# Kernel optimization log

Measured on AMD Instinct MI355X. Metric: run time of the kernel, lower is better.

The kernel has to match this reference:

```python
import jax, jax.numpy as jnp
import numpy as np

N_ORDER = 256
BATCH = 512
SEQ_LEN = 4096


def make_legs_matrices(N):
    # HiPPO-LegS: A[n,k] = -sqrt(2n+1)sqrt(2k+1) for n>k, -(n+1) for n==k, 0 for n<k
    # B[n] = sqrt(2n+1)
    q = np.arange(N, dtype=np.float64)
    r = np.sqrt(2.0 * q + 1.0)
    M = r[:, None] * r[None, :] * (q[:, None] > q[None, :]).astype(np.float64)
    M = M + np.diag(q + 1.0)
    A = -M
    B = r[:, None]
    return jnp.asarray(A, jnp.float32), jnp.asarray(B, jnp.float32)


def setup_inputs() -> dict:
    key = jax.random.key(0)
    A, Bm = make_legs_matrices(N_ORDER)
    f = jax.random.normal(key, (BATCH, SEQ_LEN), dtype=jnp.float32)
    init_state = jnp.zeros((BATCH, 1, N_ORDER), dtype=jnp.float32)
    return {"f": f, "A": A, "Bm": Bm, "init_state": init_state}


def reference(f, A, Bm, init_state):
    # Generalized bilinear transform discretization, alpha = 0.5, step = 1.0
    step = 1.0
    alpha = 0.5
    N = A.shape[0]
    I = jnp.eye(N, dtype=A.dtype)
    inv_step = 1.0 / step
    part1 = I - inv_step * alpha * A
    part2 = I + inv_step * (1.0 - alpha) * A
    # Original uses lstsq; part1 is nonsingular so solve is equivalent.
    Ad = jnp.linalg.solve(part1, part2)            # (N, N)
    Bd = jnp.linalg.solve(part1, inv_step * Bm)    # (N, 1)

    BdT = Bd.T[None]  # (1, 1, N)

    def step_fn(c, f_k):
        # c: (B, 1, N), f_k: (B,)
        # c_k = c_{k-1} @ Ad^T + Bd^T * f_k
        c = jnp.einsum('bin,mn->bim', c, Ad) + BdT * f_k[:, None, None]
        return c, None

    # scan over time axis; batch fully vectorized inside each step
    c_k, _ = jax.lax.scan(step_fn, init_state, jnp.swapaxes(f, 0, 1))
    return c_k  # (B, 1, N)
```

## Files before the change

kernel.cpp:

```cpp
#include <hip/hip_runtime.h>

#define NORD 256
#define TLEN 4096
#define NBATCH 512

__device__ __forceinline__ void fill_T2(float (*dst)[72], const float* __restrict__ s0,
                                        const float* __restrict__ s1, int stride, int t) {
  const int r = t & 63, qq = t >> 6;
  const float* p0 = s0 + (size_t)r * stride + 4 * qq;
  float4 v = *reinterpret_cast<const float4*>(p0);
  float4 w = *reinterpret_cast<const float4*>(p0 + 16);
  if (s1) {
    const float* p1 = s1 + (size_t)r * stride + 4 * qq;
    const float4 v1 = *reinterpret_cast<const float4*>(p1);
    const float4 w1 = *reinterpret_cast<const float4*>(p1 + 16);
    v.x += v1.x; v.y += v1.y; v.z += v1.z; v.w += v1.w;
    w.x += w1.x; w.y += w1.y; w.z += w1.z; w.w += w1.w;
  }
  dst[4 * qq + 0][r] = v.x;  dst[4 * qq + 1][r] = v.y;
  dst[4 * qq + 2][r] = v.z;  dst[4 * qq + 3][r] = v.w;
  dst[4 * qq + 16][r] = w.x; dst[4 * qq + 17][r] = w.y;
  dst[4 * qq + 18][r] = w.z; dst[4 * qq + 19][r] = w.w;
}

__device__ __forceinline__ void fill_N2(float (*dst)[72], const float* __restrict__ s0,
                                        const float* __restrict__ s1, int stride, int t) {
  const int kk = t >> 3, c8 = (t & 7) << 3;
  const float* p0 = s0 + (size_t)kk * stride + c8;
  float4 v = *reinterpret_cast<const float4*>(p0);
  float4 w = *reinterpret_cast<const float4*>(p0 + 4);
  if (s1) {
    const float* p1 = s1 + (size_t)kk * stride + c8;
    const float4 v1 = *reinterpret_cast<const float4*>(p1);
    const float4 w1 = *reinterpret_cast<const float4*>(p1 + 4);
    v.x += v1.x; v.y += v1.y; v.z += v1.z; v.w += v1.w;
    w.x += w1.x; w.y += w1.y; w.z += w1.z; w.w += w1.w;
  }
  dst[kk][c8 + 0] = v.x; dst[kk][c8 + 1] = v.y; dst[kk][c8 + 2] = v.z; dst[kk][c8 + 3] = v.w;
  dst[kk][c8 + 4] = w.x; dst[kk][c8 + 5] = w.y; dst[kk][c8 + 6] = w.z; dst[kk][c8 + 7] = w.w;
}

__device__ __forceinline__ void tile_fma4(const float (*As)[72], const float (*Bs)[72],
                                          int tr, int tc, float acc[4][4]) {
#pragma unroll
  for (int k = 0; k < 32; ++k) {
    const float4 a4 = *reinterpret_cast<const float4*>(&As[k][4 * tr]);
    const float4 b4 = *reinterpret_cast<const float4*>(&Bs[k][4 * tc]);
    const float a[4] = {a4.x, a4.y, a4.z, a4.w};
    const float b[4] = {b4.x, b4.y, b4.z, b4.w};
#pragma unroll
    for (int ii = 0; ii < 4; ++ii)
#pragma unroll
      for (int jj = 0; jj < 4; ++jj)
        acc[ii][jj] += a[ii] * b[jj];
  }
}

__global__ __launch_bounds__(256) void k_inv(const float* __restrict__ A,
                                             const float* __restrict__ Bm,
                                             float* __restrict__ P00, float* P01,
                                             float* __restrict__ U0, float* U1) {
  const int bid = blockIdx.x;
  const int i = threadIdx.x;
  const int wave = i >> 6, lane = i & 63;
  __shared__ float xs[NORD];
  float b = (bid < NORD) ? ((i == bid) ? 1.0f : 0.0f) : Bm[i];
  const float invd = 1.0f / (1.0f - 0.5f * A[i * NORD + i]);
  for (int w = 0; w < 4; ++w) {
    if (wave == w) {
      const int base = w << 6;
      for (int jj = 0; jj < 64; ++jj) {
        float bj = __shfl(b, jj);
        float dj = __shfl(invd, jj);
        float xj = bj * dj;
        if (lane > jj) {
          b += 0.5f * A[i * NORD + base + jj] * xj;
        } else if (lane == jj) {
          b = xj;
        }
      }
      xs[i] = b;
    }
    __syncthreads();
    if (wave > w) {
      const int base = w << 6;
      const float4* arow = reinterpret_cast<const float4*>(A + i * NORD + base);
#pragma unroll
      for (int q = 0; q < 16; ++q) {
        float4 a4 = arow[q];
        b += 0.5f * (a4.x * xs[base + 4 * q + 0] + a4.y * xs[base + 4 * q + 1] +
                     a4.z * xs[base + 4 * q + 2] + a4.w * xs[base + 4 * q + 3]);
      }
    }
  }
  if (bid < NORD) {
    P00[i * NORD + bid] = 2.0f * b - ((i == bid) ? 1.0f : 0.0f);
    if (P01) P01[(size_t)bid * 256 + i] = 0.0f;
  } else {
    U0[i] = b;
    if (U1) U1[i] = 0.0f;
  }
}

__global__ __launch_bounds__(256) void k_stage(float* U0, float* U1,
                                               const float* Pin0, const float* Pin1,
                                               float* Pout0, float* Pout1,
                                               int J, int n_apply) {
  const int bid = blockIdx.x;
  const int t = threadIdx.x;
  const int tr = t >> 4, tc = t & 15;
  __shared__ float As[32][72];
  __shared__ float Bs[32][72];
  const int kspan = U1 ? 128 : 256;

  if (bid < n_apply) {
    int work = bid, ks = 0;
    if (U1) { ks = work & 1; work >>= 1; }
    const int j0 = (work >> 2) << 6;
    const int m0 = (work & 3) << 6;
    const int klo = ks * kspan;
    float acc[4][4] = {};
    for (int kc = 0; kc < kspan; kc += 32) {
      const int k0 = klo + kc;
      fill_T2(As, U0 + (size_t)j0 * NORD + k0,
              U1 ? U1 + (size_t)j0 * NORD + k0 : nullptr, NORD, t);
      fill_T2(Bs, Pin0 + (size_t)m0 * NORD + k0,
              Pin1 ? Pin1 + (size_t)m0 * NORD + k0 : nullptr, NORD, t);
      __syncthreads();
      tile_fma4(As, Bs, tr, tc, acc);
      __syncthreads();
    }
    float* Ud = ks ? U1 : U0;
#pragma unroll
    for (int ii = 0; ii < 4; ++ii) {
      const int lr = j0 + 4 * tr + ii;
      if (lr < J) {
        float4 v = {acc[ii][0], acc[ii][1], acc[ii][2], acc[ii][3]};
        *reinterpret_cast<float4*>(&Ud[(size_t)(J + lr) * NORD + m0 + 4 * tc]) = v;
      }
    }
  } else {
    int q = bid - n_apply, ks = 0;
    if (Pin1) { ks = q & 1; q >>= 1; }
    const int m0s = (q >> 2) << 6;
    const int n0 = (q & 3) << 6;
    const int klo = ks * kspan;
    float acc[4][4] = {};
    for (int kc = 0; kc < kspan; kc += 32) {
      const int k0 = klo + kc;
      fill_T2(As, Pin0 + (size_t)m0s * NORD + k0,
              Pin1 ? Pin1 + (size_t)m0s * NORD + k0 : nullptr, NORD, t);
      fill_N2(Bs, Pin0 + (size_t)k0 * NORD + n0,
              Pin1 ? Pin1 + (size_t)k0 * NORD + n0 : nullptr, NORD, t);
      __syncthreads();
      tile_fma4(As, Bs, tr, tc, acc);
      __syncthreads();
    }
    float* Pd = ks ? Pout1 : Pout0;
#pragma unroll
    for (int ii = 0; ii < 4; ++ii) {
      float4 v = {acc[ii][0], acc[ii][1], acc[ii][2], acc[ii][3]};
      *reinterpret_cast<float4*>(&Pd[(size_t)(m0s + 4 * tr + ii) * NORD + n0 + 4 * tc]) = v;
    }
  }
}

__global__ __launch_bounds__(256) void k_final(const float* __restrict__ f,
                                               const float* __restrict__ U0,
                                               const float* U1,
                                               float* __restrict__ C) {
  const int bid = blockIdx.x;
  const int tile = bid & 15;
  const int ksf = bid >> 4;
  const int b0 = (tile >> 1) << 6;
  const int m0 = (tile & 1) << 7;
  const int k0b = ksf << 8;
  const int t = threadIdx.x;
  const int tr2 = t >> 4, tc2 = t & 15;
  __shared__ float As[32][72];
  __shared__ float Bs[32][136];
  float acc[4][8] = {};
  for (int kc = 0; kc < 256; kc += 32) {
    const int k0 = k0b + kc;
    {
      const int r = t & 63, qq = t >> 6;
      const float* p = f + (size_t)(b0 + r) * TLEN + k0 + 8 * qq;
      const float4 v = *reinterpret_cast<const float4*>(p);
      const float4 w = *reinterpret_cast<const float4*>(p + 4);
      As[8 * qq + 0][r] = v.x; As[8 * qq + 1][r] = v.y;
      As[8 * qq + 2][r] = v.z; As[8 * qq + 3][r] = v.w;
      As[8 * qq + 4][r] = w.x; As[8 * qq + 5][r] = w.y;
      As[8 * qq + 6][r] = w.z; As[8 * qq + 7][r] = w.w;
    }
    {
      const int kk = t >> 3, c16 = (t & 7) << 4;
      const size_t row = (size_t)(TLEN - 1 - (k0 + kk)) * NORD + m0 + c16;
      const float* p0 = U0 + row;
      const float* p1 = U1 ? U1 + row : nullptr;
#pragma unroll
      for (int j = 0; j < 4; ++j) {
        float4 v = *reinterpret_cast<const float4*>(p0 + 4 * j);
        if (p1) {
          const float4 w = *reinterpret_cast<const float4*>(p1 + 4 * j);
          v.x += w.x; v.y += w.y; v.z += w.z; v.w += w.w;
        }
        Bs[kk][c16 + 4 * j + 0] = v.x; Bs[kk][c16 + 4 * j + 1] = v.y;
        Bs[kk][c16 + 4 * j + 2] = v.z; Bs[kk][c16 + 4 * j + 3] = v.w;
      }
    }
    __syncthreads();
#pragma unroll
    for (int k = 0; k < 32; ++k) {
      const float4 a4 = *reinterpret_cast<const float4*>(&As[k][4 * tr2]);
      const float4 b4 = *reinterpret_cast<const float4*>(&Bs[k][8 * tc2]);
      const float4 b5 = *reinterpret_cast<const float4*>(&Bs[k][8 * tc2 + 4]);
      const float a[4] = {a4.x, a4.y, a4.z, a4.w};
      const float b[8] = {b4.x, b4.y, b4.z, b4.w, b5.x, b5.y, b5.z, b5.w};
#pragma unroll
      for (int ii = 0; ii < 4; ++ii)
#pragma unroll
        for (int jj = 0; jj < 8; ++jj)
          acc[ii][jj] += a[ii] * b[jj];
    }
    __syncthreads();
  }
#pragma unroll
  for (int ii = 0; ii < 4; ++ii)
#pragma unroll
    for (int jj = 0; jj < 8; ++jj)
      atomicAdd(&C[(size_t)(b0 + 4 * tr2 + ii) * NORD + m0 + 8 * tc2 + jj], acc[ii][jj]);
}

extern "C" void kernel_launch(void* const* d_in, const int* in_sizes, int n_in,
                              void* d_out, int out_size, void* d_ws, size_t ws_size,
                              hipStream_t stream) {
  const float* f  = (const float*)d_in[0];
  const float* A  = (const float*)d_in[1];
  const float* Bm = (const float*)d_in[2];

  float* ws = (float*)d_ws;
  const size_t need_split = (size_t)(4 * 65536 + 2 * 1048576) * sizeof(float);
  const int KS = (ws_size >= need_split) ? 2 : 1;

  float *P00, *P01, *P10, *P11, *U0, *U1;
  if (KS == 2) {
    P00 = ws;            P01 = ws + 65536;
    P10 = ws + 131072;   P11 = ws + 196608;
    U0  = ws + 262144;   U1  = U0 + 1048576;
  } else {
    P00 = ws;            P01 = nullptr;
    P10 = ws + 65536;    P11 = nullptr;
    U0  = ws + 131072;   U1  = nullptr;
  }
  float* C = (float*)d_out;

  hipMemsetAsync(d_out, 0, (size_t)NBATCH * NORD * sizeof(float), stream);

  hipLaunchKernelGGL(k_inv, dim3(NORD + 1), dim3(256), 0, stream, A, Bm, P00, P01, U0, U1);

  for (int s = 0; s < 12; ++s) {
    const int J = 1 << s;
    const float* Pin0 = (s & 1) ? P10 : P00;
    const float* Pin1 = (s & 1) ? P11 : P01;
    float* Pout0 = (s & 1) ? P00 : P10;
    float* Pout1 = (s & 1) ? P01 : P11;
    const int rtiles = (J + 63) >> 6;
    const int n_apply = (rtiles << 2) * KS;
    const int n_sq = (s < 11) ? 16 * KS : 0;
    hipLaunchKernelGGL(k_stage, dim3(n_apply + n_sq), dim3(256), 0, stream,
                       U0, U1, Pin0, Pin1, Pout0, Pout1, J, n_apply);
  }

  hipLaunchKernelGGL(k_final, dim3(256), dim3(256), 0, stream, f, U0, U1, C);
}
```

Measured before the change: 261.3 us.

## Halve impulse-response table and combine halves via final Ad^2048 multiply

The precomputed impulse response U now covers only 2048 steps instead of 4096, which drops the last doubling stage. The final contraction splits the sequence into two halves. The early half is accumulated into a scratch buffer and then multiplied by Ad^2048 in a new combine kernel before being added to the output. Shared-memory tile loaders are also rewritten for coalesced row reads with padding 68. The change adds an extra memset, an extra kernel launch and more atomics in exchange for less U generation and memory traffic.

```diff
diff --git a/kernel.cpp b/kernel.cpp
--- a/kernel.cpp
+++ b/kernel.cpp
@@ -2,45 +2,11 @@
 
 #define NORD 256
 #define TLEN 4096
+#define HTLEN 2048
 #define NBATCH 512
 
-__device__ __forceinline__ void fill_T2(float (*dst)[72], const float* __restrict__ s0,
-                                        const float* __restrict__ s1, int stride, int t) {
-  const int r = t & 63, qq = t >> 6;
-  const float* p0 = s0 + (size_t)r * stride + 4 * qq;
-  float4 v = *reinterpret_cast<const float4*>(p0);
-  float4 w = *reinterpret_cast<const float4*>(p0 + 16);
-  if (s1) {
-    const float* p1 = s1 + (size_t)r * stride + 4 * qq;
-    const float4 v1 = *reinterpret_cast<const float4*>(p1);
-    const float4 w1 = *reinterpret_cast<const float4*>(p1 + 16);
-    v.x += v1.x; v.y += v1.y; v.z += v1.z; v.w += v1.w;
-    w.x += w1.x; w.y += w1.y; w.z += w1.z; w.w += w1.w;
-  }
-  dst[4 * qq + 0][r] = v.x;  dst[4 * qq + 1][r] = v.y;
-  dst[4 * qq + 2][r] = v.z;  dst[4 * qq + 3][r] = v.w;
-  dst[4 * qq + 16][r] = w.x; dst[4 * qq + 17][r] = w.y;
-  dst[4 * qq + 18][r] = w.z; dst[4 * qq + 19][r] = w.w;
-}
-
-__device__ __forceinline__ void fill_N2(float (*dst)[72], const float* __restrict__ s0,
-                                        const float* __restrict__ s1, int stride, int t) {
-  const int kk = t >> 3, c8 = (t & 7) << 3;
-  const float* p0 = s0 + (size_t)kk * stride + c8;
-  float4 v = *reinterpret_cast<const float4*>(p0);
-  float4 w = *reinterpret_cast<const float4*>(p0 + 4);
-  if (s1) {
-    const float* p1 = s1 + (size_t)kk * stride + c8;
-    const float4 v1 = *reinterpret_cast<const float4*>(p1);
-    const float4 w1 = *reinterpret_cast<const float4*>(p1 + 4);
-    v.x += v1.x; v.y += v1.y; v.z += v1.z; v.w += v1.w;
-    w.x += w1.x; w.y += w1.y; w.z += w1.z; w.w += w1.w;
-  }
-  dst[kk][c8 + 0] = v.x; dst[kk][c8 + 1] = v.y; dst[kk][c8 + 2] = v.z; dst[kk][c8 + 3] = v.w;
-  dst[kk][c8 + 4] = w.x; dst[kk][c8 + 5] = w.y; dst[kk][c8 + 6] = w.z; dst[kk][c8 + 7] = w.w;
-}
-
-__device__ __forceinline__ void tile_fma4(const float (*As)[72], const float (*Bs)[72],
+
+__device__ __forceinline__ void tile_fma4(const float (*As)[68], const float (*Bs)[68],
                                           int tr, int tc, float acc[4][4]) {
 #pragma unroll
   for (int k = 0; k < 32; ++k) {
@@ -53,6 +19,23 @@
 #pragma unroll
       for (int jj = 0; jj < 4; ++jj)
         acc[ii][jj] += a[ii] * b[jj];
+  }
+}
+
+__device__ __forceinline__ void fill_tr(float (*dst)[68], const float* __restrict__ s0,
+                                        const float* __restrict__ s1,
+                                        int row0, int stride, int k0, int t) {
+  const int rr = t >> 3, cc = (t & 7) << 2;
+#pragma unroll
+  for (int p = 0; p < 64; p += 32) {
+    const size_t off = (size_t)(row0 + rr + p) * stride + k0 + cc;
+    float4 v = *reinterpret_cast<const float4*>(s0 + off);
+    if (s1) {
+      const float4 w = *reinterpret_cast<const float4*>(s1 + off);
+      v.x += w.x; v.y += w.y; v.z += w.z; v.w += w.w;
+    }
+    dst[cc + 0][rr + p] = v.x; dst[cc + 1][rr + p] = v.y;
+    dst[cc + 2][rr + p] = v.z; dst[cc + 3][rr + p] = v.w;
   }
 }
 
@@ -109,8 +92,8 @@
   const int bid = blockIdx.x;
   const int t = threadIdx.x;
   const int tr = t >> 4, tc = t & 15;
-  __shared__ float As[32][72];
-  __shared__ float Bs[32][72];
+  __shared__ float As[32][68];
+  __shared__ float Bs[32][68];
   const int kspan = U1 ? 128 : 256;
 
   if (bid < n_apply) {
@@ -122,10 +105,8 @@
     float acc[4][4] = {};
     for (int kc = 0; kc < kspan; kc += 32) {
       const int k0 = klo + kc;
-      fill_T2(As, U0 + (size_t)j0 * NORD + k0,
-              U1 ? U1 + (size_t)j0 * NORD + k0 : nullptr, NORD, t);
-      fill_T2(Bs, Pin0 + (size_t)m0 * NORD + k0,
-              Pin1 ? Pin1 + (size_t)m0 * NORD + k0 : nullptr, NORD, t);
+      fill_tr(As, U0, U1, j0, NORD, k0, t);
+      fill_tr(Bs, Pin0, Pin1, m0, NORD, k0, t);
       __syncthreads();
       tile_fma4(As, Bs, tr, tc, acc);
       __syncthreads();
@@ -145,13 +126,21 @@
     const int m0s = (q >> 2) << 6;
     const int n0 = (q & 3) << 6;
     const int klo = ks * kspan;
+    const int rr = t >> 3, cc = (t & 7) << 2;
     float acc[4][4] = {};
     for (int kc = 0; kc < kspan; kc += 32) {
       const int k0 = klo + kc;
-      fill_T2(As, Pin0 + (size_t)m0s * NORD + k0,
-              Pin1 ? Pin1 + (size_t)m0s * NORD + k0 : nullptr, NORD, t);
-      fill_N2(Bs, Pin0 + (size_t)k0 * NORD + n0,
-              Pin1 ? Pin1 + (size_t)k0 * NORD + n0 : nullptr, NORD, t);
+      fill_tr(As, Pin0, Pin1, m0s, NORD, k0, t);
+#pragma unroll
+      for (int p = 0; p < 64; p += 32) {
+        const size_t off = (size_t)(k0 + rr) * NORD + n0 + cc + p;
+        float4 v = *reinterpret_cast<const float4*>(Pin0 + off);
+        if (Pin1) {
+          const float4 w = *reinterpret_cast<const float4*>(Pin1 + off);
+          v.x += w.x; v.y += w.y; v.z += w.z; v.w += w.w;
+        }
+        *reinterpret_cast<float4*>(&Bs[rr][cc + p]) = v;
+      }
       __syncthreads();
       tile_fma4(As, Bs, tr, tc, acc);
       __syncthreads();
@@ -168,52 +157,50 @@
 __global__ __launch_bounds__(256) void k_final(const float* __restrict__ f,
                                                const float* __restrict__ U0,
                                                const float* U1,
+                                               float* __restrict__ Glow,
                                                float* __restrict__ C) {
   const int bid = blockIdx.x;
-  const int tile = bid & 15;
-  const int ksf = bid >> 4;
-  const int b0 = (tile >> 1) << 6;
-  const int m0 = (tile & 1) << 7;
-  const int k0b = ksf << 8;
+  const int tile = bid & 31, ksf = bid >> 5;
+  const int rt = tile >> 1, ct = tile & 1;
+  const int h = rt >> 3;
+  const int b0 = (rt & 7) << 6;
+  const int m0 = ct << 7;
+  const int jbase = ksf << 7;
   const int t = threadIdx.x;
-  const int tr2 = t >> 4, tc2 = t & 15;
-  __shared__ float As[32][72];
-  __shared__ float Bs[32][136];
+  const int tr = t >> 4, tc = t & 15;
+  __shared__ float As[32][68];
+  __shared__ float Bs0[32][68];
+  __shared__ float Bs1[32][68];
+  const int rr = t >> 3, cc = (t & 7) << 2;
+  const int jr = t >> 5, c32 = t & 31;
   float acc[4][8] = {};
-  for (int kc = 0; kc < 256; kc += 32) {
-    const int k0 = k0b + kc;
-    {
-      const int r = t & 63, qq = t >> 6;
-      const float* p = f + (size_t)(b0 + r) * TLEN + k0 + 8 * qq;
-      const float4 v = *reinterpret_cast<const float4*>(p);
-      const float4 w = *reinterpret_cast<const float4*>(p + 4);
-      As[8 * qq + 0][r] = v.x; As[8 * qq + 1][r] = v.y;
-      As[8 * qq + 2][r] = v.z; As[8 * qq + 3][r] = v.w;
-      As[8 * qq + 4][r] = w.x; As[8 * qq + 5][r] = w.y;
-      As[8 * qq + 6][r] = w.z; As[8 * qq + 7][r] = w.w;
-    }
-    {
-      const int kk = t >> 3, c16 = (t & 7) << 4;
-      const size_t row = (size_t)(TLEN - 1 - (k0 + kk)) * NORD + m0 + c16;
-      const float* p0 = U0 + row;
-      const float* p1 = U1 ? U1 + row : nullptr;
-#pragma unroll
-      for (int j = 0; j < 4; ++j) {
-        float4 v = *reinterpret_cast<const float4*>(p0 + 4 * j);
-        if (p1) {
-          const float4 w = *reinterpret_cast<const float4*>(p1 + 4 * j);
-          v.x += w.x; v.y += w.y; v.z += w.z; v.w += w.w;
-        }
-        Bs[kk][c16 + 4 * j + 0] = v.x; Bs[kk][c16 + 4 * j + 1] = v.y;
-        Bs[kk][c16 + 4 * j + 2] = v.z; Bs[kk][c16 + 4 * j + 3] = v.w;
-      }
+  for (int kc = 0; kc < 128; kc += 32) {
+    const int j0 = jbase + kc;
+#pragma unroll
+    for (int p = 0; p < 64; p += 32) {
+      const float4 v = *reinterpret_cast<const float4*>(
+          f + (size_t)(b0 + rr + p) * TLEN + HTLEN * h + j0 + cc);
+      As[cc + 0][rr + p] = v.x; As[cc + 1][rr + p] = v.y;
+      As[cc + 2][rr + p] = v.z; As[cc + 3][rr + p] = v.w;
+    }
+#pragma unroll
+    for (int p = 0; p < 32; p += 8) {
+      const int jj = jr + p;
+      const size_t off = (size_t)(HTLEN - 1 - (j0 + jj)) * NORD + m0 + 4 * c32;
+      float4 v = *reinterpret_cast<const float4*>(U0 + off);
+      if (U1) {
+        const float4 w = *reinterpret_cast<const float4*>(U1 + off);
+        v.x += w.x; v.y += w.y; v.z += w.z; v.w += w.w;
+      }
+      if (c32 < 16) *reinterpret_cast<float4*>(&Bs0[jj][4 * c32]) = v;
+      else          *reinterpret_cast<float4*>(&Bs1[jj][4 * (c32 - 16)]) = v;
     }
     __syncthreads();
 #pragma unroll
     for (int k = 0; k < 32; ++k) {
-      const float4 a4 = *reinterpret_cast<const float4*>(&As[k][4 * tr2]);
-      const float4 b4 = *reinterpret_cast<const float4*>(&Bs[k][8 * tc2]);
-      const float4 b5 = *reinterpret_cast<const float4*>(&Bs[k][8 * tc2 + 4]);
+      const float4 a4 = *reinterpret_cast<const float4*>(&As[k][4 * tr]);
+      const float4 b4 = *reinterpret_cast<const float4*>(&Bs0[k][4 * tc]);
+      const float4 b5 = *reinterpret_cast<const float4*>(&Bs1[k][4 * tc]);
       const float a[4] = {a4.x, a4.y, a4.z, a4.w};
       const float b[8] = {b4.x, b4.y, b4.z, b4.w, b5.x, b5.y, b5.z, b5.w};
 #pragma unroll
@@ -224,11 +211,44 @@
     }
     __syncthreads();
   }
+  float* dst = h ? C : Glow;
+#pragma unroll
+  for (int ii = 0; ii < 4; ++ii) {
+    const int row = b0 + 4 * tr + ii;
+#pragma unroll
+    for (int jj = 0; jj < 8; ++jj) {
+      const int col = m0 + ((jj < 4) ? (4 * tc + jj) : (64 + 4 * tc + (jj - 4)));
+      atomicAdd(dst + (size_t)row * NORD + col, acc[ii][jj]);
+    }
+  }
+}
+
+__global__ __launch_bounds__(256) void k_combine(const float* __restrict__ Glow,
+                                                 const float* __restrict__ P0,
+                                                 const float* P1,
+                                                 float* __restrict__ C) {
+  const int bid = blockIdx.x;
+  const int b0 = (bid >> 2) << 6;
+  const int m0 = (bid & 3) << 6;
+  const int t = threadIdx.x;
+  const int tr = t >> 4, tc = t & 15;
+  __shared__ float As[32][68];
+  __shared__ float Bs[32][68];
+  float acc[4][4] = {};
+  for (int k0 = 0; k0 < NORD; k0 += 32) {
+    fill_tr(As, Glow, nullptr, b0, NORD, k0, t);
+    fill_tr(Bs, P0, P1, m0, NORD, k0, t);
+    __syncthreads();
+    tile_fma4(As, Bs, tr, tc, acc);
+    __syncthreads();
+  }
 #pragma unroll
   for (int ii = 0; ii < 4; ++ii)
 #pragma unroll
-    for (int jj = 0; jj < 8; ++jj)
-      atomicAdd(&C[(size_t)(b0 + 4 * tr2 + ii) * NORD + m0 + 8 * tc2 + jj], acc[ii][jj]);
+    for (int jj = 0; jj < 4; ++jj) {
+      float* p = C + (size_t)(b0 + 4 * tr + ii) * NORD + m0 + 4 * tc + jj;
+      *p += acc[ii][jj];
+    }
 }
 
 extern "C" void kernel_launch(void* const* d_in, const int* in_sizes, int n_in,
@@ -239,26 +259,29 @@
   const float* Bm = (const float*)d_in[2];
 
   float* ws = (float*)d_ws;
-  const size_t need_split = (size_t)(4 * 65536 + 2 * 1048576) * sizeof(float);
+  const size_t need_split = (size_t)(4 * 65536 + 2 * 524288 + 131072) * sizeof(float);
   const int KS = (ws_size >= need_split) ? 2 : 1;
 
-  float *P00, *P01, *P10, *P11, *U0, *U1;
+  float *P00, *P01, *P10, *P11, *U0, *U1, *Glow;
   if (KS == 2) {
     P00 = ws;            P01 = ws + 65536;
     P10 = ws + 131072;   P11 = ws + 196608;
-    U0  = ws + 262144;   U1  = U0 + 1048576;
+    U0  = ws + 262144;   U1  = U0 + 524288;
+    Glow = U0 + 1048576;
   } else {
     P00 = ws;            P01 = nullptr;
     P10 = ws + 65536;    P11 = nullptr;
     U0  = ws + 131072;   U1  = nullptr;
+    Glow = ws + 655360;
   }
   float* C = (float*)d_out;
 
   hipMemsetAsync(d_out, 0, (size_t)NBATCH * NORD * sizeof(float), stream);
+  hipMemsetAsync(Glow, 0, (size_t)NBATCH * NORD * sizeof(float), stream);
 
   hipLaunchKernelGGL(k_inv, dim3(NORD + 1), dim3(256), 0, stream, A, Bm, P00, P01, U0, U1);
 
-  for (int s = 0; s < 12; ++s) {
+  for (int s = 0; s <= 10; ++s) {
     const int J = 1 << s;
     const float* Pin0 = (s & 1) ? P10 : P00;
     const float* Pin1 = (s & 1) ? P11 : P01;
@@ -266,10 +289,11 @@
     float* Pout1 = (s & 1) ? P01 : P11;
     const int rtiles = (J + 63) >> 6;
     const int n_apply = (rtiles << 2) * KS;
-    const int n_sq = (s < 11) ? 16 * KS : 0;
+    const int n_sq = 16 * KS;
     hipLaunchKernelGGL(k_stage, dim3(n_apply + n_sq), dim3(256), 0, stream,
                        U0, U1, Pin0, Pin1, Pout0, Pout1, J, n_apply);
   }
 
-  hipLaunchKernelGGL(k_final, dim3(256), dim3(256), 0, stream, f, U0, U1, C);
-}
+  hipLaunchKernelGGL(k_final, dim3(512), dim3(256), 0, stream, f, U0, U1, Glow, C);
+  hipLaunchKernelGGL(k_combine, dim3(32), dim3(256), 0, stream, Glow, P10, P11, C);
+}
```

Result: no change. 259.9 us (-0.5%).
